# Kernel optimization log

Hardware: AMD Instinct MI355X
Metric: run time of the kernel (lower is better)

The kernel has to match this reference:

```python
import jax, jax.numpy as jnp
import numpy as np

D_MODEL, H, D_FF = 1024, 16, 4096
D_K = D_MODEL // H
EPS = 1e-5


def _layernorm(x, alpha, bias):
    # faithful to source: unbiased std (ddof=1), eps added to std (not var)
    mean = jnp.mean(x, axis=-1, keepdims=True)
    std = jnp.std(x, axis=-1, keepdims=True, ddof=1)
    return alpha * (x - mean) / (std + EPS) + bias


def setup_inputs() -> dict:
    key = jax.random.key(0)
    ks = jax.random.split(key, 12)
    B, S = 2, 2048
    s = 1.0 / np.sqrt(D_MODEL)
    inp = {
        "x": jax.random.normal(ks[0], (B, S, D_MODEL), dtype=jnp.float32),
        "mask": jnp.ones((B, 1, 1, S), dtype=jnp.int32),
        "wq": jax.random.normal(ks[1], (D_MODEL, D_MODEL), dtype=jnp.float32) * s,
        "wk": jax.random.normal(ks[2], (D_MODEL, D_MODEL), dtype=jnp.float32) * s,
        "wv": jax.random.normal(ks[3], (D_MODEL, D_MODEL), dtype=jnp.float32) * s,
        "wo": jax.random.normal(ks[4], (D_MODEL, D_MODEL), dtype=jnp.float32) * s,
        "w1": jax.random.normal(ks[5], (D_MODEL, D_FF), dtype=jnp.float32) * s,
        "b1": jnp.zeros((D_FF,), dtype=jnp.float32),
        "w2": jax.random.normal(ks[6], (D_FF, D_MODEL), dtype=jnp.float32) * (1.0 / np.sqrt(D_FF)),
        "b2": jnp.zeros((D_MODEL,), dtype=jnp.float32),
        "alpha1": jnp.ones((1,), dtype=jnp.float32),
        "bias1": jnp.zeros((1,), dtype=jnp.float32),
        "alpha2": jnp.ones((1,), dtype=jnp.float32),
        "bias2": jnp.zeros((1,), dtype=jnp.float32),
    }
    return inp


def reference(x, mask, wq, wk, wv, wo, w1, b1, w2, b2, alpha1, bias1, alpha2, bias2):
    B, S, _ = x.shape

    # --- sublayer 1: pre-norm self-attention + residual ---
    xn = _layernorm(x, alpha1, bias1)
    q = (xn @ wq).reshape(B, S, H, D_K).transpose(0, 2, 1, 3)  # [B,H,S,Dk]
    k = (xn @ wk).reshape(B, S, H, D_K).transpose(0, 2, 1, 3)
    v = (xn @ wv).reshape(B, S, H, D_K).transpose(0, 2, 1, 3)

    scores = jnp.einsum("bhqd,bhkd->bhqk", q, k) / np.sqrt(D_K)  # [B,H,S,S]
    scores = jnp.where(mask == 0, jnp.float32(-1e9), scores)
    attn = jax.nn.softmax(scores, axis=-1)
    ctx = jnp.einsum("bhqk,bhkd->bhqd", attn, v)
    ctx = ctx.transpose(0, 2, 1, 3).reshape(B, S, D_MODEL)
    x = x + ctx @ wo

    # --- sublayer 2: pre-norm FFN + residual ---
    xn = _layernorm(x, alpha2, bias2)
    h = jax.nn.relu(xn @ w1 + b1)
    x = x + h @ w2 + b2
    return x
```

## Files before the change

kernel.cpp:

```cpp
#include <hip/hip_runtime.h>
#include <hip/hip_bf16.h>

typedef __attribute__((ext_vector_type(8))) short bf16x8;
typedef __attribute__((ext_vector_type(4))) short short4v;
typedef __attribute__((ext_vector_type(4))) float floatx4;

#define MFMA16(A, B, C) __builtin_amdgcn_mfma_f32_16x16x32_bf16((A), (B), (C), 0, 0, 0)

__device__ inline short bf16bits(float f) {
  __hip_bfloat16 h = __float2bfloat16(f);
  return *reinterpret_cast<short*>(&h);
}
__device__ inline unsigned cvtpk(float lo, float hi) {
  unsigned r;
  asm("v_cvt_pk_bf16_f32 %0, %1, %2" : "=v"(r) : "v"(lo), "v"(hi));
  return r;
}
typedef __attribute__((address_space(3))) char lds_char;
typedef __attribute__((address_space(1))) const char glob_char;
__device__ inline void gll16(const void* g, void* l) {
  __builtin_amdgcn_global_load_lds((glob_char*)g, (lds_char*)l, 16, 0, 0);
}

__global__ __launch_bounds__(256) void ln_qkvtrans_kernel(
    const float* __restrict__ x, __hip_bfloat16* __restrict__ y,
    const float* __restrict__ alpha_p, const float* __restrict__ bias_p,
    const float* __restrict__ wq, const float* __restrict__ wk,
    const float* __restrict__ wv, __hip_bfloat16* __restrict__ wqkvT) {
  __shared__ __align__(16) __hip_bfloat16 tile[64][72];
  const int bid = blockIdx.x;
  const int t = threadIdx.x;
  if (bid < 1024) {
    const int wvv = t >> 6, lane = t & 63;
    const long row = (long)bid * 4 + wvv;
    const float* xr = x + row * 1024;
    float4 v4[4];
#pragma unroll
    for (int i = 0; i < 4; i++) v4[i] = *(const float4*)&xr[lane * 4 + i * 256];
    float sum = 0.f, sq = 0.f;
#pragma unroll
    for (int i = 0; i < 4; i++) {
      sum += (v4[i].x + v4[i].y) + (v4[i].z + v4[i].w);
      sq += (v4[i].x * v4[i].x + v4[i].y * v4[i].y) +
            (v4[i].z * v4[i].z + v4[i].w * v4[i].w);
    }
#pragma unroll
    for (int off = 32; off; off >>= 1) {
      sum += __shfl_xor(sum, off);
      sq += __shfl_xor(sq, off);
    }
    const float mean = sum * (1.f / 1024.f);
    float var = (sq - 1024.f * mean * mean) * (1.f / 1023.f);
    var = fmaxf(var, 0.f);
    const float denom = sqrtf(var) + 1e-5f;
    const float sc = alpha_p[0] / denom;
    const float beta = bias_p[0];
    __hip_bfloat16* yr = y + row * 1024;
#pragma unroll
    for (int i = 0; i < 4; i++) {
      uint2 st;
      st.x = cvtpk((v4[i].x - mean) * sc + beta, (v4[i].y - mean) * sc + beta);
      st.y = cvtpk((v4[i].z - mean) * sc + beta, (v4[i].w - mean) * sc + beta);
      *(uint2*)&yr[lane * 4 + i * 256] = st;
    }
  } else {
    const int tt = bid - 1024;
    const int which = tt >> 8;
    const float* src = which == 0 ? wq : (which == 1 ? wk : wv);
    __hip_bfloat16* dst = wqkvT + (size_t)which * 1024 * 1024;
    const long r0 = (long)((tt >> 4) & 15) * 64, c0 = (long)(tt & 15) * 64;
    for (int i = t; i < 1024; i += 256) {
      int r = i >> 4, c4 = (i & 15) * 4;
      float4 f = *(const float4*)&src[(r0 + r) * 1024 + c0 + c4];
      short4v s;
      s[0] = bf16bits(f.x); s[1] = bf16bits(f.y);
      s[2] = bf16bits(f.z); s[3] = bf16bits(f.w);
      *(short4v*)&tile[r][c4] = s;
    }
    __syncthreads();
    for (int i = t; i < 512; i += 256) {
      int c = i >> 3, r8 = (i & 7) * 8;
      bf16x8 sv;
#pragma unroll
      for (int j = 0; j < 8; j++) sv[j] = *reinterpret_cast<const short*>(&tile[r8 + j][c]);
      *(bf16x8*)&dst[(c0 + c) * 1024 + r0 + r8] = sv;
    }
  }
}

__global__ __launch_bounds__(256) void prep_kernel(
    const __hip_bfloat16* __restrict__ qkv, __hip_bfloat16* __restrict__ vt,
    const float* __restrict__ wo, __hip_bfloat16* __restrict__ woT,
    const int* __restrict__ mask, float* __restrict__ addm,
    int* __restrict__ flags) {
  __shared__ __align__(16) __hip_bfloat16 tile[64][72];
  __shared__ int ok[4];
  const int bid = blockIdx.x;
  if (bid < 1024) {
    const int bh = bid >> 5, b = bh >> 4, h = bh & 15;
    const long s0 = (long)(bid & 31) * 64;
    const __hip_bfloat16* src = qkv + ((long)b * 2048 + s0) * 3072 + 2048 + h * 64;
    for (int i = threadIdx.x; i < 512; i += 256) {
      int s = i >> 3, d8 = (i & 7) * 8;
      *(uint4*)&tile[s][d8] = *(const uint4*)&src[(long)s * 3072 + d8];
    }
    __syncthreads();
    __hip_bfloat16* dstb = vt + (long)bh * 64 * 2048 + s0;
    for (int i = threadIdx.x; i < 512; i += 256) {
      int d = i >> 3, s8 = (i & 7) * 8;
      bf16x8 sv;
#pragma unroll
      for (int j = 0; j < 8; j++) sv[j] = *reinterpret_cast<const short*>(&tile[s8 + j][d]);
      *(bf16x8*)&dstb[(long)d * 2048 + s8] = sv;
    }
  } else if (bid < 1280) {
    const int t = bid - 1024;
    const long r0 = (long)(t >> 4) * 64, c0 = (long)(t & 15) * 64;
    for (int i = threadIdx.x; i < 1024; i += 256) {
      int r = i >> 4, c4 = (i & 15) * 4;
      float4 f = *(const float4*)&wo[(r0 + r) * 1024 + c0 + c4];
      short4v s;
      s[0] = bf16bits(f.x); s[1] = bf16bits(f.y);
      s[2] = bf16bits(f.z); s[3] = bf16bits(f.w);
      *(short4v*)&tile[r][c4] = s;
    }
    __syncthreads();
    for (int i = threadIdx.x; i < 512; i += 256) {
      int c = i >> 3, r8 = (i & 7) * 8;
      bf16x8 sv;
#pragma unroll
      for (int j = 0; j < 8; j++) sv[j] = *reinterpret_cast<const short*>(&tile[r8 + j][c]);
      *(bf16x8*)&woT[(c0 + c) * 1024 + r0 + r8] = sv;
    }
  } else {
    const int i = (bid - 1280) * 256 + threadIdx.x;
    const int mv = mask[i];
    addm[i] = mv ? 0.f : -1e30f;
    const unsigned long long bal = __ballot(mv != 0);
    if ((threadIdx.x & 63) == 0) ok[threadIdx.x >> 6] = (bal == ~0ull) ? 1 : 0;
    __syncthreads();
    if (threadIdx.x == 0) flags[bid - 1280] = ok[0] & ok[1] & ok[2] & ok[3];
  }
}

__global__ __launch_bounds__(256) void ln2_wtrans_kernel(
    const float* __restrict__ x1, __hip_bfloat16* __restrict__ xn2,
    const float* __restrict__ alpha_p, const float* __restrict__ bias_p,
    const float* __restrict__ w1c, const float* __restrict__ w2c,
    __hip_bfloat16* __restrict__ w1Th, __hip_bfloat16* __restrict__ w2Th) {
  __shared__ __align__(16) __hip_bfloat16 tile[64][72];
  const int bid = blockIdx.x;
  const int t = threadIdx.x;
  if (bid < 1024) {
    const int wvv = t >> 6, lane = t & 63;
    const long row = (long)bid * 4 + wvv;
    const float* xr = x1 + row * 1024;
    float4 v4[4];
#pragma unroll
    for (int i = 0; i < 4; i++) v4[i] = *(const float4*)&xr[lane * 4 + i * 256];
    float sum = 0.f, sq = 0.f;
#pragma unroll
    for (int i = 0; i < 4; i++) {
      sum += (v4[i].x + v4[i].y) + (v4[i].z + v4[i].w);
      sq += (v4[i].x * v4[i].x + v4[i].y * v4[i].y) +
            (v4[i].z * v4[i].z + v4[i].w * v4[i].w);
    }
#pragma unroll
    for (int off = 32; off; off >>= 1) {
      sum += __shfl_xor(sum, off);
      sq += __shfl_xor(sq, off);
    }
    const float mean = sum * (1.f / 1024.f);
    float var = (sq - 1024.f * mean * mean) * (1.f / 1023.f);
    var = fmaxf(var, 0.f);
    const float denom = sqrtf(var) + 1e-5f;
    const float sc = alpha_p[0] / denom;
    const float beta = bias_p[0];
    __hip_bfloat16* yr = xn2 + row * 1024;
#pragma unroll
    for (int i = 0; i < 4; i++) {
      uint2 st;
      st.x = cvtpk((v4[i].x - mean) * sc + beta, (v4[i].y - mean) * sc + beta);
      st.y = cvtpk((v4[i].z - mean) * sc + beta, (v4[i].w - mean) * sc + beta);
      *(uint2*)&yr[lane * 4 + i * 256] = st;
    }
  } else {
    const int wb = bid - 1024;
    const float* src;
    __hip_bfloat16* dst;
    int R, ldS;
    long r0, c0;
    if (wb < 512) {
      src = w1c; dst = w1Th; R = 1024; ldS = 4096;
      r0 = (long)(wb >> 5) * 64; c0 = (long)(wb & 31) * 64;
    } else {
      const int t2 = wb - 512;
      src = w2c; dst = w2Th; R = 2048; ldS = 1024;
      r0 = (long)(t2 >> 4) * 64; c0 = (long)(t2 & 15) * 64;
    }
    for (int i = t; i < 1024; i += 256) {
      int r = i >> 4, c4 = (i & 15) * 4;
      float4 f = *(const float4*)&src[(r0 + r) * ldS + c0 + c4];
      short4v s;
      s[0] = bf16bits(f.x); s[1] = bf16bits(f.y);
      s[2] = bf16bits(f.z); s[3] = bf16bits(f.w);
      *(short4v*)&tile[r][c4] = s;
    }
    __syncthreads();
    for (int i = t; i < 512; i += 256) {
      int c = i >> 3, r8 = (i & 7) * 8;
      bf16x8 sv;
#pragma unroll
      for (int j = 0; j < 8; j++) sv[j] = *reinterpret_cast<const short*>(&tile[r8 + j][c]);
      *(bf16x8*)&dst[(c0 + c) * R + r0 + r8] = sv;
    }
  }
}

__global__ __launch_bounds__(256) void wtrans_kernel(
    const float* __restrict__ w1c, const float* __restrict__ w2c,
    __hip_bfloat16* __restrict__ w1Th, __hip_bfloat16* __restrict__ w2Th) {
  __shared__ __align__(16) __hip_bfloat16 tile[64][72];
  const int bid = blockIdx.x;
  const float* src;
  __hip_bfloat16* dst;
  int R, ldS;
  long r0, c0;
  if (bid < 512) {
    src = w1c; dst = w1Th; R = 1024; ldS = 4096;
    r0 = (long)(bid >> 5) * 64; c0 = (long)(bid & 31) * 64;
  } else {
    const int t = bid - 512;
    src = w2c; dst = w2Th; R = 2048; ldS = 1024;
    r0 = (long)(t >> 4) * 64; c0 = (long)(t & 15) * 64;
  }
  for (int i = threadIdx.x; i < 1024; i += 256) {
    int r = i >> 4, c4 = (i & 15) * 4;
    float4 f = *(const float4*)&src[(r0 + r) * ldS + c0 + c4];
    short4v s;
    s[0] = bf16bits(f.x); s[1] = bf16bits(f.y);
    s[2] = bf16bits(f.z); s[3] = bf16bits(f.w);
    *(short4v*)&tile[r][c4] = s;
  }
  __syncthreads();
  for (int i = threadIdx.x; i < 512; i += 256) {
    int c = i >> 3, r8 = (i & 7) * 8;
    bf16x8 sv;
#pragma unroll
    for (int j = 0; j < 8; j++) sv[j] = *reinterpret_cast<const short*>(&tile[r8 + j][c]);
    *(bf16x8*)&dst[(c0 + c) * R + r0 + r8] = sv;
  }
}

__global__ __launch_bounds__(256) void bias_add_kernel(
    const float* __restrict__ x1, const float* __restrict__ b2,
    float* __restrict__ out) {
  const int i = (blockIdx.x * 256 + threadIdx.x) * 4;
  float4 v = *(const float4*)&x1[i];
  const float4 bb = *(const float4*)&b2[i & 1023];
  v.x += bb.x; v.y += bb.y; v.z += bb.z; v.w += bb.w;
  *(float4*)&out[i] = v;
}

template <int EPI>
__global__ __launch_bounds__(256) void gemm_bt_kernel(
    const __hip_bfloat16* __restrict__ A, const __hip_bfloat16* __restrict__ Bt,
    void* __restrict__ Cv, const float* __restrict__ bias,
    const float* __restrict__ res, int M, int N, int K) {
  __shared__ __align__(16) __hip_bfloat16 lA[2][128 * 32];
  __shared__ __align__(16) __hip_bfloat16 lB[2][128 * 32];
  const int tid = threadIdx.x;
  const int wave = tid >> 6, lane = tid & 63;
  const int quad = lane >> 4, l16 = lane & 15;
  const int wm = wave >> 1, wn = wave & 1;

  const int gx = gridDim.x;
  const int nwg = gx * gridDim.y;
  int bid = blockIdx.y * gx + blockIdx.x;
  bid = (bid & 7) * (nwg >> 3) + (bid >> 3);
  const long m0 = (long)(bid / gx) * 128;
  const long n0 = (long)(bid % gx) * 128;

  const int rA0 = tid >> 2, cA0 = (tid & 3) * 8;
  const int rA1 = (tid + 256) >> 2, cA1 = ((tid + 256) & 3) * 8;

  floatx4 acc[4][4];
#pragma unroll
  for (int i = 0; i < 4; i++)
#pragma unroll
    for (int j = 0; j < 4; j++) acc[i][j] = (floatx4){0.f, 0.f, 0.f, 0.f};

  const __hip_bfloat16* Ab = A + m0 * K;
  const __hip_bfloat16* Bb = Bt + n0 * K;

  gll16(&Ab[(long)rA0 * K + cA0], &lA[0][wave * 512]);
  gll16(&Ab[(long)rA1 * K + cA1], &lA[0][2048 + wave * 512]);
  gll16(&Bb[(long)rA0 * K + cA0], &lB[0][wave * 512]);
  gll16(&Bb[(long)rA1 * K + cA1], &lB[0][2048 + wave * 512]);

  int cur = 0;
  for (int k0 = 0; k0 < K; k0 += 32) {
    __syncthreads();
    if (k0 + 32 < K) {
      const int nxt = cur ^ 1;
      gll16(&Ab[(long)rA0 * K + k0 + 32 + cA0], &lA[nxt][wave * 512]);
      gll16(&Ab[(long)rA1 * K + k0 + 32 + cA1], &lA[nxt][2048 + wave * 512]);
      gll16(&Bb[(long)rA0 * K + k0 + 32 + cA0], &lB[nxt][wave * 512]);
      gll16(&Bb[(long)rA1 * K + k0 + 32 + cA1], &lB[nxt][2048 + wave * 512]);
    }
    bf16x8 af[4], bfr[4];
#pragma unroll
    for (int mi = 0; mi < 4; mi++)
      af[mi] = *(const bf16x8*)&lA[cur][(wm * 64 + mi * 16 + l16) * 32 + quad * 8];
#pragma unroll
    for (int ni = 0; ni < 4; ni++)
      bfr[ni] = *(const bf16x8*)&lB[cur][(wn * 64 + ni * 16 + l16) * 32 + quad * 8];
#pragma unroll
    for (int mi = 0; mi < 4; mi++)
#pragma unroll
      for (int ni = 0; ni < 4; ni++)
        acc[mi][ni] = MFMA16(af[mi], bfr[ni], acc[mi][ni]);
    cur ^= 1;
  }

#pragma unroll
  for (int mi = 0; mi < 4; mi++) {
#pragma unroll
    for (int ni = 0; ni < 4; ni++) {
#pragma unroll
      for (int r = 0; r < 4; r++) {
        const long row = m0 + wm * 64 + mi * 16 + quad * 4 + r;
        const long col = n0 + wn * 64 + ni * 16 + l16;
        const long idx = row * N + col;
        float v = acc[mi][ni][r];
        if (EPI == 0) {
          ((__hip_bfloat16*)Cv)[idx] = __float2bfloat16(v);
        } else if (EPI == 1) {
          ((float*)Cv)[idx] = v + res[idx];
        } else if (EPI == 2) {
          v += bias[col];
          ((__hip_bfloat16*)Cv)[idx] = __float2bfloat16(fmaxf(v, 0.f));
        } else if (EPI == 3) {
          float* Cf = (float*)Cv;
          Cf[idx] = Cf[idx] + v;
        }
      }
    }
  }
}

template <int EPI>
__global__ __launch_bounds__(256) void gemm_bt_k64_kernel(
    const __hip_bfloat16* __restrict__ A, const __hip_bfloat16* __restrict__ Bt,
    void* __restrict__ Cv, const float* __restrict__ bias,
    const float* __restrict__ res, int M, int N, int K) {
  __shared__ __align__(16) __hip_bfloat16 lA[2][128 * 64];
  __shared__ __align__(16) __hip_bfloat16 lB[2][128 * 64];
  const int tid = threadIdx.x;
  const int wave = tid >> 6, lane = tid & 63;
  const int quad = lane >> 4, l16 = lane & 15;
  const int wm = wave >> 1, wn = wave & 1;

  const int gx = gridDim.x;
  const int nwg = gx * gridDim.y;
  int bid = blockIdx.y * gx + blockIdx.x;
  bid = (bid & 7) * (nwg >> 3) + (bid >> 3);
  const long m0 = (long)(bid / gx) * 128;
  const long n0 = (long)(bid % gx) * 128;

  const int srow = lane >> 3;
  const int cg = (lane & 7) ^ srow;

  floatx4 acc[4][4];
#pragma unroll
  for (int i = 0; i < 4; i++)
#pragma unroll
    for (int j = 0; j < 4; j++) acc[i][j] = (floatx4){0.f, 0.f, 0.f, 0.f};

  const __hip_bfloat16* Ab = A + m0 * K;
  const __hip_bfloat16* Bb = Bt + n0 * K;

#pragma unroll
  for (int j = 0; j < 4; ++j) {
    const int c = wave + j * 4;
    gll16(&Ab[(long)(c * 8 + srow) * K + cg * 8], &lA[0][c * 512]);
    gll16(&Bb[(long)(c * 8 + srow) * K + cg * 8], &lB[0][c * 512]);
  }

  int cur = 0;
  for (int k0 = 0; k0 < K; k0 += 64) {
    __syncthreads();
    if (k0 + 64 < K) {
      const int nxt = cur ^ 1;
#pragma unroll
      for (int j = 0; j < 4; ++j) {
        const int c = wave + j * 4;
        gll16(&Ab[(long)(c * 8 + srow) * K + k0 + 64 + cg * 8], &lA[nxt][c * 512]);
        gll16(&Bb[(long)(c * 8 + srow) * K + k0 + 64 + cg * 8], &lB[nxt][c * 512]);
      }
    }
#pragma unroll
    for (int ks = 0; ks < 2; ++ks) {
      bf16x8 af[4], bfr[4];
#pragma unroll
      for (int mi = 0; mi < 4; mi++) {
        const int row = wm * 64 + mi * 16 + l16;
        af[mi] = *(const bf16x8*)&lA[cur][row * 64 +
                                          (((ks * 4 + quad) ^ (l16 & 7)) * 8)];
      }
#pragma unroll
      for (int ni = 0; ni < 4; ni++) {
        const int row = wn * 64 + ni * 16 + l16;
        bfr[ni] = *(const bf16x8*)&lB[cur][row * 64 +
                                           (((ks * 4 + quad) ^ (l16 & 7)) * 8)];
      }
#pragma unroll
      for (int mi = 0; mi < 4; mi++)
#pragma unroll
        for (int ni = 0; ni < 4; ni++)
          acc[mi][ni] = MFMA16(af[mi], bfr[ni], acc[mi][ni]);
    }
    cur ^= 1;
  }

#pragma unroll
  for (int mi = 0; mi < 4; mi++) {
#pragma unroll
    for (int ni = 0; ni < 4; ni++) {
#pragma unroll
      for (int r = 0; r < 4; r++) {
        const long row = m0 + wm * 64 + mi * 16 + quad * 4 + r;
        const long col = n0 + wn * 64 + ni * 16 + l16;
        const long idx = row * N + col;
        float v = acc[mi][ni][r];
        if (EPI == 0) {
          ((__hip_bfloat16*)Cv)[idx] = __float2bfloat16(v);
        } else if (EPI == 1) {
          ((float*)Cv)[idx] = v + res[idx];
        } else if (EPI == 2) {
          v += bias[col];
          ((__hip_bfloat16*)Cv)[idx] = __float2bfloat16(fmaxf(v, 0.f));
        } else if (EPI == 3) {
          float* Cf = (float*)Cv;
          Cf[idx] = Cf[idx] + v;
        }
      }
    }
  }
}

template <int EPI>
__global__ __launch_bounds__(256) void gemm64_bt_kernel(
    const __hip_bfloat16* __restrict__ A, const __hip_bfloat16* __restrict__ Bt,
    void* __restrict__ Cv, const float* __restrict__ bias,
    const float* __restrict__ res, int M, int N, int K) {
  __shared__ __align__(16) __hip_bfloat16 lA[2][128 * 64];
  __shared__ __align__(16) __hip_bfloat16 lB[2][64 * 64];
  const int tid = threadIdx.x;
  const int wave = tid >> 6, lane = tid & 63;
  const int quad = lane >> 4, l16 = lane & 15;
  const int wm = wave >> 1, wn = wave & 1;

  const int gx = gridDim.x;
  const int nwg = gx * gridDim.y;
  int bid = blockIdx.y * gx + blockIdx.x;
  bid = (bid & 7) * (nwg >> 3) + (bid >> 3);
  const long m0 = (long)(bid / gx) * 128;
  const long n0 = (long)(bid % gx) * 64;

  const int srow = lane >> 3;
  const int cg = (lane & 7) ^ srow;

  floatx4 acc[4][2];
#pragma unroll
  for (int i = 0; i < 4; i++)
#pragma unroll
    for (int j = 0; j < 2; j++) acc[i][j] = (floatx4){0.f, 0.f, 0.f, 0.f};

  const __hip_bfloat16* Ab = A + m0 * K;
  const __hip_bfloat16* Bb = Bt + n0 * K;

#pragma unroll
  for (int j = 0; j < 4; ++j) {
    const int c = wave + j * 4;
    gll16(&Ab[(long)(c * 8 + srow) * K + cg * 8], &lA[0][c * 512]);
  }
#pragma unroll
  for (int j = 0; j < 2; ++j) {
    const int c = wave + j * 4;
    gll16(&Bb[(long)(c * 8 + srow) * K + cg * 8], &lB[0][c * 512]);
  }

  int cur = 0;
  for (int k0 = 0; k0 < K; k0 += 64) {
    __syncthreads();
    if (k0 + 64 < K) {
      const int nxt = cur ^ 1;
#pragma unroll
      for (int j = 0; j < 4; ++j) {
        const int c = wave + j * 4;
        gll16(&Ab[(long)(c * 8 + srow) * K + k0 + 64 + cg * 8], &lA[nxt][c * 512]);
      }
#pragma unroll
      for (int j = 0; j < 2; ++j) {
        const int c = wave + j * 4;
        gll16(&Bb[(long)(c * 8 + srow) * K + k0 + 64 + cg * 8], &lB[nxt][c * 512]);
      }
    }
#pragma unroll
    for (int ks = 0; ks < 2; ++ks) {
      bf16x8 af[4], bfr[2];
#pragma unroll
      for (int mi = 0; mi < 4; mi++) {
        const int row = wm * 64 + mi * 16 + l16;
        af[mi] = *(const bf16x8*)&lA[cur][row * 64 +
                                          (((ks * 4 + quad) ^ (l16 & 7)) * 8)];
      }
#pragma unroll
      for (int ni = 0; ni < 2; ni++) {
        const int row = wn * 32 + ni * 16 + l16;
        bfr[ni] = *(const bf16x8*)&lB[cur][row * 64 +
                                           (((ks * 4 + quad) ^ (l16 & 7)) * 8)];
      }
#pragma unroll
      for (int mi = 0; mi < 4; mi++)
#pragma unroll
        for (int ni = 0; ni < 2; ni++)
          acc[mi][ni] = MFMA16(af[mi], bfr[ni], acc[mi][ni]);
    }
    cur ^= 1;
  }

#pragma unroll
  for (int mi = 0; mi < 4; mi++) {
#pragma unroll
    for (int ni = 0; ni < 2; ni++) {
#pragma unroll
      for (int r = 0; r < 4; r++) {
        const long row = m0 + wm * 64 + mi * 16 + quad * 4 + r;
        const long col = n0 + wn * 32 + ni * 16 + l16;
        const long idx = row * N + col;
        float v = acc[mi][ni][r];
        if (EPI == 1) {
          ((float*)Cv)[idx] = v + res[idx];
        } else if (EPI == 3) {
          float* Cf = (float*)Cv;
          Cf[idx] = Cf[idx] + v;
        }
      }
    }
  }
}

__global__ __launch_bounds__(256) void attn_kernel(
    const __hip_bfloat16* __restrict__ qkv, const __hip_bfloat16* __restrict__ vt,
    const float* __restrict__ addm, const int* __restrict__ flags,
    __hip_bfloat16* __restrict__ ctx) {
  __shared__ __align__(16) __hip_bfloat16 lK[2][64 * 64];
  __shared__ __align__(16) __hip_bfloat16 lV[3][64 * 64];
  __shared__ __align__(16) __hip_bfloat16 lP[4][16 * 64];
  const int tid = threadIdx.x, wave = tid >> 6, lane = tid & 63;
  const int quad = lane >> 4, l16 = lane & 15;
  const int nwg = gridDim.x * gridDim.y;
  int bid0 = blockIdx.y * gridDim.x + blockIdx.x;
  bid0 = (bid0 & 7) * (nwg >> 3) + (bid0 >> 3);
  const int bh = bid0 >> 5, b = bh >> 4, h = bh & 15;
  const int q0 = (bid0 & 31) * 64 + wave * 16;
  const float cs = 0.18033688011112042f;
  const float inv_cs = 5.545177444479562f;

  const __hip_bfloat16* kb = qkv + (long)b * 2048 * 3072 + 1024 + h * 64;
  const __hip_bfloat16* vb = vt + (long)bh * 64 * 2048;
  const float* am = addm + b * 2048;

  int fm = 1;
#pragma unroll
  for (int i = 0; i < 8; ++i) fm &= flags[b * 8 + i];
  const bool fast = (fm != 0);

  const long qoff = ((long)b * 2048 + q0 + l16) * 3072 + h * 64;
  const bf16x8 bq0 = *(const bf16x8*)&qkv[qoff + quad * 8];
  const bf16x8 bq1 = *(const bf16x8*)&qkv[qoff + 32 + quad * 8];

  const int srow = lane >> 3;
  const int cslot = lane & 7;
  const int cg = cslot ^ srow;
  const int rbase = wave * 16 + srow;

  char* const pbase = (char*)&lP[wave][0];
  const int prow = l16 * 128;
  const int pswz = l16 & 7;

  floatx4 o[4];
#pragma unroll
  for (int mi = 0; mi < 4; mi++) o[mi] = (floatx4){0.f, 0.f, 0.f, 0.f};
  float mrow = 10.0f, lrow = 0.f;
  float rs_prev = 0.f, tms_prev = -3.0e38f;

#pragma unroll
  for (int j = 0; j < 2; ++j) {
    const int rloc = rbase + j * 8;
    gll16(kb + (long)rloc * 3072 + cg * 8, &lK[0][(wave * 16 + j * 8) * 64]);
    gll16(vb + (long)rloc * 2048 + cg * 8, &lV[0][(wave * 16 + j * 8) * 64]);
  }

  int kcur = 0;
  int vN = 1;
  int vP = 2;
  for (int t = 0; t <= 32; ++t) {
    __syncthreads();
    if (t + 1 < 32) {
      const int knxt = kcur ^ 1;
#pragma unroll
      for (int j = 0; j < 2; ++j) {
        const int rloc = rbase + j * 8;
        gll16(kb + (long)((t + 1) * 64 + rloc) * 3072 + cg * 8,
              &lK[knxt][(wave * 16 + j * 8) * 64]);
        gll16(vb + (long)rloc * 2048 + (t + 1) * 64 + cg * 8,
              &lV[vN][(wave * 16 + j * 8) * 64]);
      }
    }

    if (t >= 1) {
      const __hip_bfloat16* lVp = lV[vP];
#pragma unroll
      for (int ss = 0; ss < 2; ++ss) {
        const bf16x8 bp = *(const bf16x8*)(pbase + prow +
                                           ((((ss << 2) + quad) ^ pswz) << 4));
        __builtin_amdgcn_s_setprio(1);
#pragma unroll
        for (int mi = 0; mi < 4; ++mi) {
          const bf16x8 av = *(const bf16x8*)&lVp[(mi * 16 + l16) * 64 +
                                                 ((ss * 4 + quad) ^ (l16 & 7)) * 8];
          o[mi] = MFMA16(av, bp, o[mi]);
        }
        __builtin_amdgcn_s_setprio(0);
      }
      lrow += rs_prev;
      if (__any(tms_prev > mrow + 8.f)) {
        const float mnew = fmaxf(mrow, tms_prev);
        const float alpha = __builtin_amdgcn_exp2f(mrow - mnew);
        mrow = mnew;
        lrow *= alpha;
#pragma unroll
        for (int mi = 0; mi < 4; mi++) o[mi] *= alpha;
      }
    }

    if (t < 32) {
      const __hip_bfloat16* lKc = lK[kcur];
      floatx4 c[4];
      __builtin_amdgcn_s_setprio(1);
#pragma unroll
      for (int g = 0; g < 4; ++g) {
        const bf16x8 a0 =
            *(const bf16x8*)&lKc[(g * 16 + l16) * 64 + ((quad) ^ (l16 & 7)) * 8];
        const bf16x8 a1 =
            *(const bf16x8*)&lKc[(g * 16 + l16) * 64 + ((4 + quad) ^ (l16 & 7)) * 8];
        floatx4 cc = {0.f, 0.f, 0.f, 0.f};
        cc = MFMA16(a0, bq0, cc);
        cc = MFMA16(a1, bq1, cc);
        c[g] = cc;
      }
      __builtin_amdgcn_s_setprio(0);

      if (!fast) {
#pragma unroll
        for (int g = 0; g < 4; ++g) {
          const float4 a4 = *(const float4*)&am[t * 64 + g * 16 + quad * 4];
          c[g][0] = fmaf(a4.x, inv_cs, c[g][0]);
          c[g][1] = fmaf(a4.y, inv_cs, c[g][1]);
          c[g][2] = fmaf(a4.z, inv_cs, c[g][2]);
          c[g][3] = fmaf(a4.w, inv_cs, c[g][3]);
        }
      }

      const float mneg = -mrow;
      float p[4][4];
#pragma unroll
      for (int g = 0; g < 4; ++g)
#pragma unroll
        for (int r = 0; r < 4; ++r)
          p[g][r] = __builtin_amdgcn_exp2f(fmaf(c[g][r], cs, mneg));

#pragma unroll
      for (int g = 0; g < 4; ++g) {
        uint2 w2;
        w2.x = cvtpk(p[g][0], p[g][1]);
        w2.y = cvtpk(p[g][2], p[g][3]);
        const int slot16 = (g * 2 + (quad >> 1)) ^ pswz;
        *(uint2*)(pbase + prow + (slot16 << 4) + ((quad & 1) << 3)) = w2;
      }

      const float m0 = fmaxf(fmaxf(c[0][0], c[0][1]), c[0][2]);
      const float m1 = fmaxf(fmaxf(c[0][3], c[1][0]), c[1][1]);
      const float m2 = fmaxf(fmaxf(c[1][2], c[1][3]), c[2][0]);
      const float m3 = fmaxf(fmaxf(c[2][1], c[2][2]), c[2][3]);
      const float m4 = fmaxf(fmaxf(c[3][0], c[3][1]), c[3][2]);
      float tm = fmaxf(fmaxf(fmaxf(m0, m1), fmaxf(m2, m3)), fmaxf(m4, c[3][3]));
      tm = fmaxf(tm, __shfl_xor(tm, 16));
      tm = fmaxf(tm, __shfl_xor(tm, 32));
      tms_prev = tm * cs;

      const float s0 = (p[0][0] + p[0][1]) + (p[0][2] + p[0][3]);
      const float s1 = (p[1][0] + p[1][1]) + (p[1][2] + p[1][3]);
      const float s2 = (p[2][0] + p[2][1]) + (p[2][2] + p[2][3]);
      const float s3 = (p[3][0] + p[3][1]) + (p[3][2] + p[3][3]);
      float rs = (s0 + s1) + (s2 + s3);
      rs += __shfl_xor(rs, 16);
      rs += __shfl_xor(rs, 32);
      rs_prev = rs;
    }

    kcur ^= 1;
    vN = (vN == 2) ? 0 : vN + 1;
    vP = (vP == 2) ? 0 : vP + 1;
  }

  const float inv_l = 1.f / lrow;
  const long cb = ((long)b * 2048 + q0 + l16) * 1024 + h * 64;
#pragma unroll
  for (int mi = 0; mi < 4; mi++) {
    uint2 st;
    st.x = cvtpk(o[mi][0] * inv_l, o[mi][1] * inv_l);
    st.y = cvtpk(o[mi][2] * inv_l, o[mi][3] * inv_l);
    *(uint2*)&ctx[cb + mi * 16 + quad * 4] = st;
  }
}

extern "C" void kernel_launch(void* const* d_in, const int* in_sizes, int n_in,
                              void* d_out, int out_size, void* d_ws, size_t ws_size,
                              hipStream_t stream) {
  const float* x = (const float*)d_in[0];
  const int* mask = (const int*)d_in[1];
  const float* wq = (const float*)d_in[2];
  const float* wk = (const float*)d_in[3];
  const float* wv = (const float*)d_in[4];
  const float* wo = (const float*)d_in[5];
  const float* w1 = (const float*)d_in[6];
  const float* b1 = (const float*)d_in[7];
  const float* w2 = (const float*)d_in[8];
  const float* b2 = (const float*)d_in[9];
  const float* alpha1 = (const float*)d_in[10];
  const float* bias1 = (const float*)d_in[11];
  const float* alpha2 = (const float*)d_in[12];
  const float* bias2 = (const float*)d_in[13];

  char* ws = (char*)d_ws;
  char* dob = (char*)d_out;
  const size_t MiB = 1048576;
  __hip_bfloat16* qkv   = (__hip_bfloat16*)(ws + 0);
  __hip_bfloat16* wqkvT = (__hip_bfloat16*)(ws + 24 * MiB);
  __hip_bfloat16* vtb   = (__hip_bfloat16*)(ws + 24 * MiB);
  float*          x1    = (float*)(ws + 0);
  __hip_bfloat16* hc    = (__hip_bfloat16*)(ws + 16 * MiB);
  __hip_bfloat16* xn    = (__hip_bfloat16*)d_out;
  __hip_bfloat16* ctxb  = (__hip_bfloat16*)d_out;
  __hip_bfloat16* xn2   = (__hip_bfloat16*)d_out;
  __hip_bfloat16* woT   = (__hip_bfloat16*)(dob + 8 * MiB);
  __hip_bfloat16* w1Th  = (__hip_bfloat16*)(dob + 8 * MiB);
  __hip_bfloat16* w2Th  = (__hip_bfloat16*)(dob + 12 * MiB);
  float*          addm  = (float*)(dob + 12 * MiB);
  int*            flags = (int*)(dob + 12 * MiB + 16 * 1024);

  const dim3 b256(256);
  ln_qkvtrans_kernel<<<1792, b256, 0, stream>>>(x, xn, alpha1, bias1,
                                                wq, wk, wv, wqkvT);
  gemm_bt_kernel<0><<<dim3(24, 32), b256, 0, stream>>>(xn, wqkvT, qkv, nullptr,
                                                       nullptr, 4096, 3072, 1024);
  prep_kernel<<<1296, b256, 0, stream>>>(qkv, vtb, wo, woT, mask, addm, flags);
  attn_kernel<<<dim3(32, 32), b256, 0, stream>>>(qkv, vtb, addm, flags, ctxb);
  gemm64_bt_kernel<1><<<dim3(16, 32), b256, 0, stream>>>(ctxb, woT, x1, nullptr, x,
                                                         4096, 1024, 1024);
  ln2_wtrans_kernel<<<2048, b256, 0, stream>>>(x1, xn2, alpha2, bias2,
                                               w1, w2, w1Th, w2Th);
  gemm_bt_k64_kernel<2><<<dim3(16, 32), b256, 0, stream>>>(xn2, w1Th, hc,
                                                           b1, nullptr,
                                                           4096, 2048, 1024);
  gemm64_bt_kernel<3><<<dim3(16, 32), b256, 0, stream>>>(hc, w2Th, x1, nullptr,
                                                         nullptr, 4096, 1024, 2048);
  wtrans_kernel<<<1024, b256, 0, stream>>>(w1 + 2048,
                                           w2 + (size_t)2048 * 1024,
                                           w1Th, w2Th);
  gemm_bt_k64_kernel<2><<<dim3(16, 32), b256, 0, stream>>>(xn2, w1Th, hc,
                                                           b1 + 2048, nullptr,
                                                           4096, 2048, 1024);
  gemm64_bt_kernel<3><<<dim3(16, 32), b256, 0, stream>>>(hc, w2Th, x1, nullptr,
                                                         nullptr, 4096, 1024, 2048);
  bias_add_kernel<<<4096, b256, 0, stream>>>(x1, b2, (float*)d_out);
}
```

Measured before the change: 401.4 us.

## Remove skewed PV pipelining in attention and shrink V buffers to double

Restructures the flash-attention loop so the P·V MFMA for a tile runs in the same iteration as its QK scores and softmax, instead of one iteration later. V staging drops from three LDS buffers to two, sharing the K double-buffer index, and the rescale is applied immediately. This simplifies control flow and reduces LDS use, which may raise occupancy. The cost is the cross-iteration overlap between the PV matmul and the next tile's score and exponent work.

```diff
diff --git a/kernel.cpp b/kernel.cpp
--- a/kernel.cpp
+++ b/kernel.cpp
@@ -557,7 +557,7 @@
     const float* __restrict__ addm, const int* __restrict__ flags,
     __hip_bfloat16* __restrict__ ctx) {
   __shared__ __align__(16) __hip_bfloat16 lK[2][64 * 64];
-  __shared__ __align__(16) __hip_bfloat16 lV[3][64 * 64];
+  __shared__ __align__(16) __hip_bfloat16 lV[2][64 * 64];
   __shared__ __align__(16) __hip_bfloat16 lP[4][16 * 64];
   const int tid = threadIdx.x, wave = tid >> 6, lane = tid & 63;
   const int quad = lane >> 4, l16 = lane & 15;
@@ -595,7 +595,6 @@
 #pragma unroll
   for (int mi = 0; mi < 4; mi++) o[mi] = (floatx4){0.f, 0.f, 0.f, 0.f};
   float mrow = 10.0f, lrow = 0.f;
-  float rs_prev = 0.f, tms_prev = -3.0e38f;
 
 #pragma unroll
   for (int j = 0; j < 2; ++j) {
@@ -604,117 +603,108 @@
     gll16(vb + (long)rloc * 2048 + cg * 8, &lV[0][(wave * 16 + j * 8) * 64]);
   }
 
-  int kcur = 0;
-  int vN = 1;
-  int vP = 2;
-  for (int t = 0; t <= 32; ++t) {
+  int cur = 0;
+  for (int t = 0; t < 32; ++t) {
     __syncthreads();
     if (t + 1 < 32) {
-      const int knxt = kcur ^ 1;
+      const int nxt = cur ^ 1;
 #pragma unroll
       for (int j = 0; j < 2; ++j) {
         const int rloc = rbase + j * 8;
         gll16(kb + (long)((t + 1) * 64 + rloc) * 3072 + cg * 8,
-              &lK[knxt][(wave * 16 + j * 8) * 64]);
+              &lK[nxt][(wave * 16 + j * 8) * 64]);
         gll16(vb + (long)rloc * 2048 + (t + 1) * 64 + cg * 8,
-              &lV[vN][(wave * 16 + j * 8) * 64]);
-      }
-    }
-
-    if (t >= 1) {
-      const __hip_bfloat16* lVp = lV[vP];
-#pragma unroll
-      for (int ss = 0; ss < 2; ++ss) {
-        const bf16x8 bp = *(const bf16x8*)(pbase + prow +
-                                           ((((ss << 2) + quad) ^ pswz) << 4));
-        __builtin_amdgcn_s_setprio(1);
-#pragma unroll
-        for (int mi = 0; mi < 4; ++mi) {
-          const bf16x8 av = *(const bf16x8*)&lVp[(mi * 16 + l16) * 64 +
-                                                 ((ss * 4 + quad) ^ (l16 & 7)) * 8];
-          o[mi] = MFMA16(av, bp, o[mi]);
-        }
-        __builtin_amdgcn_s_setprio(0);
-      }
-      lrow += rs_prev;
-      if (__any(tms_prev > mrow + 8.f)) {
-        const float mnew = fmaxf(mrow, tms_prev);
-        const float alpha = __builtin_amdgcn_exp2f(mrow - mnew);
-        mrow = mnew;
-        lrow *= alpha;
-#pragma unroll
-        for (int mi = 0; mi < 4; mi++) o[mi] *= alpha;
-      }
-    }
-
-    if (t < 32) {
-      const __hip_bfloat16* lKc = lK[kcur];
-      floatx4 c[4];
+              &lV[nxt][(wave * 16 + j * 8) * 64]);
+      }
+    }
+    const __hip_bfloat16* lKc = lK[cur];
+    const __hip_bfloat16* lVc = lV[cur];
+
+    floatx4 c[4];
+    __builtin_amdgcn_s_setprio(1);
+#pragma unroll
+    for (int g = 0; g < 4; ++g) {
+      const bf16x8 a0 =
+          *(const bf16x8*)&lKc[(g * 16 + l16) * 64 + ((quad) ^ (l16 & 7)) * 8];
+      const bf16x8 a1 =
+          *(const bf16x8*)&lKc[(g * 16 + l16) * 64 + ((4 + quad) ^ (l16 & 7)) * 8];
+      floatx4 cc = {0.f, 0.f, 0.f, 0.f};
+      cc = MFMA16(a0, bq0, cc);
+      cc = MFMA16(a1, bq1, cc);
+      c[g] = cc;
+    }
+    __builtin_amdgcn_s_setprio(0);
+
+    if (!fast) {
+#pragma unroll
+      for (int g = 0; g < 4; ++g) {
+        const float4 a4 = *(const float4*)&am[t * 64 + g * 16 + quad * 4];
+        c[g][0] = fmaf(a4.x, inv_cs, c[g][0]);
+        c[g][1] = fmaf(a4.y, inv_cs, c[g][1]);
+        c[g][2] = fmaf(a4.z, inv_cs, c[g][2]);
+        c[g][3] = fmaf(a4.w, inv_cs, c[g][3]);
+      }
+    }
+
+    const float mneg = -mrow;
+    float p[4][4];
+#pragma unroll
+    for (int g = 0; g < 4; ++g)
+#pragma unroll
+      for (int r = 0; r < 4; ++r)
+        p[g][r] = __builtin_amdgcn_exp2f(fmaf(c[g][r], cs, mneg));
+
+#pragma unroll
+    for (int g = 0; g < 4; ++g) {
+      uint2 w2;
+      w2.x = cvtpk(p[g][0], p[g][1]);
+      w2.y = cvtpk(p[g][2], p[g][3]);
+      const int slot16 = (g * 2 + (quad >> 1)) ^ pswz;
+      *(uint2*)(pbase + prow + (slot16 << 4) + ((quad & 1) << 3)) = w2;
+    }
+
+    const float m0 = fmaxf(fmaxf(c[0][0], c[0][1]), c[0][2]);
+    const float m1 = fmaxf(fmaxf(c[0][3], c[1][0]), c[1][1]);
+    const float m2 = fmaxf(fmaxf(c[1][2], c[1][3]), c[2][0]);
+    const float m3 = fmaxf(fmaxf(c[2][1], c[2][2]), c[2][3]);
+    const float m4 = fmaxf(fmaxf(c[3][0], c[3][1]), c[3][2]);
+    float tm = fmaxf(fmaxf(fmaxf(m0, m1), fmaxf(m2, m3)), fmaxf(m4, c[3][3]));
+    tm = fmaxf(tm, __shfl_xor(tm, 16));
+    tm = fmaxf(tm, __shfl_xor(tm, 32));
+    const float tms = tm * cs;
+
+    const float s0 = (p[0][0] + p[0][1]) + (p[0][2] + p[0][3]);
+    const float s1 = (p[1][0] + p[1][1]) + (p[1][2] + p[1][3]);
+    const float s2 = (p[2][0] + p[2][1]) + (p[2][2] + p[2][3]);
+    const float s3 = (p[3][0] + p[3][1]) + (p[3][2] + p[3][3]);
+    float rs = (s0 + s1) + (s2 + s3);
+    rs += __shfl_xor(rs, 16);
+    rs += __shfl_xor(rs, 32);
+
+#pragma unroll
+    for (int ss = 0; ss < 2; ++ss) {
+      const bf16x8 bp = *(const bf16x8*)(pbase + prow +
+                                         ((((ss << 2) + quad) ^ pswz) << 4));
       __builtin_amdgcn_s_setprio(1);
 #pragma unroll
-      for (int g = 0; g < 4; ++g) {
-        const bf16x8 a0 =
-            *(const bf16x8*)&lKc[(g * 16 + l16) * 64 + ((quad) ^ (l16 & 7)) * 8];
-        const bf16x8 a1 =
-            *(const bf16x8*)&lKc[(g * 16 + l16) * 64 + ((4 + quad) ^ (l16 & 7)) * 8];
-        floatx4 cc = {0.f, 0.f, 0.f, 0.f};
-        cc = MFMA16(a0, bq0, cc);
-        cc = MFMA16(a1, bq1, cc);
-        c[g] = cc;
+      for (int mi = 0; mi < 4; ++mi) {
+        const bf16x8 av = *(const bf16x8*)&lVc[(mi * 16 + l16) * 64 +
+                                               ((ss * 4 + quad) ^ (l16 & 7)) * 8];
+        o[mi] = MFMA16(av, bp, o[mi]);
       }
       __builtin_amdgcn_s_setprio(0);
-
-      if (!fast) {
-#pragma unroll
-        for (int g = 0; g < 4; ++g) {
-          const float4 a4 = *(const float4*)&am[t * 64 + g * 16 + quad * 4];
-          c[g][0] = fmaf(a4.x, inv_cs, c[g][0]);
-          c[g][1] = fmaf(a4.y, inv_cs, c[g][1]);
-          c[g][2] = fmaf(a4.z, inv_cs, c[g][2]);
-          c[g][3] = fmaf(a4.w, inv_cs, c[g][3]);
-        }
-      }
-
-      const float mneg = -mrow;
-      float p[4][4];
-#pragma unroll
-      for (int g = 0; g < 4; ++g)
-#pragma unroll
-        for (int r = 0; r < 4; ++r)
-          p[g][r] = __builtin_amdgcn_exp2f(fmaf(c[g][r], cs, mneg));
-
-#pragma unroll
-      for (int g = 0; g < 4; ++g) {
-        uint2 w2;
-        w2.x = cvtpk(p[g][0], p[g][1]);
-        w2.y = cvtpk(p[g][2], p[g][3]);
-        const int slot16 = (g * 2 + (quad >> 1)) ^ pswz;
-        *(uint2*)(pbase + prow + (slot16 << 4) + ((quad & 1) << 3)) = w2;
-      }
-
-      const float m0 = fmaxf(fmaxf(c[0][0], c[0][1]), c[0][2]);
-      const float m1 = fmaxf(fmaxf(c[0][3], c[1][0]), c[1][1]);
-      const float m2 = fmaxf(fmaxf(c[1][2], c[1][3]), c[2][0]);
-      const float m3 = fmaxf(fmaxf(c[2][1], c[2][2]), c[2][3]);
-      const float m4 = fmaxf(fmaxf(c[3][0], c[3][1]), c[3][2]);
-      float tm = fmaxf(fmaxf(fmaxf(m0, m1), fmaxf(m2, m3)), fmaxf(m4, c[3][3]));
-      tm = fmaxf(tm, __shfl_xor(tm, 16));
-      tm = fmaxf(tm, __shfl_xor(tm, 32));
-      tms_prev = tm * cs;
-
-      const float s0 = (p[0][0] + p[0][1]) + (p[0][2] + p[0][3]);
-      const float s1 = (p[1][0] + p[1][1]) + (p[1][2] + p[1][3]);
-      const float s2 = (p[2][0] + p[2][1]) + (p[2][2] + p[2][3]);
-      const float s3 = (p[3][0] + p[3][1]) + (p[3][2] + p[3][3]);
-      float rs = (s0 + s1) + (s2 + s3);
-      rs += __shfl_xor(rs, 16);
-      rs += __shfl_xor(rs, 32);
-      rs_prev = rs;
-    }
-
-    kcur ^= 1;
-    vN = (vN == 2) ? 0 : vN + 1;
-    vP = (vP == 2) ? 0 : vP + 1;
+    }
+
+    lrow += rs;
+    if (__any(tms > mrow + 8.f)) {
+      const float mnew = fmaxf(mrow, tms);
+      const float alpha = __builtin_amdgcn_exp2f(mrow - mnew);
+      mrow = mnew;
+      lrow *= alpha;
+#pragma unroll
+      for (int mi = 0; mi < 4; mi++) o[mi] *= alpha;
+    }
+    cur ^= 1;
   }
 
   const float inv_l = 1.f / lrow;
```

Result: faster. 380.7 us (-5.2%).
